# Performance work log

Hardware: AMD Instinct MI355X
Metric: run time of the kernel (lower is better)

## Reference

```python
import jax, jax.numpy as jnp
import numpy as np

ROW = 48   # num_row_points
COL = 48   # num_column_points
K = 21     # kernel_size


def _grid_sample_translate(ker, tx, ty):
    """Bilinear grid_sample (zeros padding, align_corners=True) for a pure
    per-image translation grid. ker: [N, h, w]; tx, ty: [N] normalized shifts.
    Matches F.affine_grid(identity + translation) + F.grid_sample."""
    N, h, w = ker.shape
    dt = ker.dtype
    # source pixel coords: px = x_out + tx*(w-1)/2 (align_corners=True)
    px = jnp.arange(w, dtype=dt)[None, :] + tx[:, None] * (w - 1) / 2  # [N, w]
    py = jnp.arange(h, dtype=dt)[None, :] + ty[:, None] * (h - 1) / 2  # [N, h]

    x0 = jnp.floor(px); fx = px - x0
    def gat_w(i):
        m = ((i >= 0) & (i <= w - 1)).astype(dt)
        ic = jnp.clip(i, 0, w - 1).astype(jnp.int32)
        v = jnp.take_along_axis(ker, jnp.broadcast_to(ic[:, None, :], ker.shape), axis=2)
        return v * m[:, None, :]
    gx = gat_w(x0) * (1 - fx)[:, None, :] + gat_w(x0 + 1) * fx[:, None, :]

    y0 = jnp.floor(py); fy = py - y0
    def gat_h(i):
        m = ((i >= 0) & (i <= h - 1)).astype(dt)
        ic = jnp.clip(i, 0, h - 1).astype(jnp.int32)
        v = jnp.take_along_axis(gx, jnp.broadcast_to(ic[:, :, None], gx.shape), axis=1)
        return v * m[:, :, None]
    return gat_h(y0) * (1 - fy)[:, :, None] + gat_h(y0 + 1) * fy[:, :, None]


def setup_inputs() -> dict:
    key = jax.random.key(0)
    k1, k2, k3 = jax.random.split(key, 3)
    N = ROW * COL
    inp = jax.random.normal(k1, (4, 64, 192, 192), dtype=jnp.float32)
    # torch.rand init; floor at 0.05 to avoid a degenerate zero sigma draw
    sigma_x = jax.random.uniform(k2, (N,), dtype=jnp.float32, minval=0.05, maxval=1.0)
    sigma_y = jax.random.uniform(k3, (N,), dtype=jnp.float32, minval=0.05, maxval=1.0)
    opacity = jnp.ones((N, 1), dtype=jnp.float32)
    return {"inp": inp, "sigma_x": sigma_x, "sigma_y": sigma_y, "opacity": opacity}


def reference(inp, sigma_x, sigma_y, opacity):
    B, C, H, W = inp.shape
    nbr, nbc = H // ROW, W // COL
    L = nbr * nbc
    N = ROW * COL

    # Unfold into non-overlapping ROWxCOL patches -> [B*L, C, ROW, COL]
    patches = (inp.reshape(B, C, nbr, ROW, nbc, COL)
                  .transpose(0, 2, 4, 1, 3, 5)
                  .reshape(B * L, C, ROW, COL))
    colors = patches.reshape(B * L, C, N).transpose(0, 2, 1)  # [BL, N, C]

    # meshgrid point coords: index k = i*COL + j, x=j (col), y=i (row)
    ii, jj = jnp.meshgrid(jnp.arange(ROW), jnp.arange(COL), indexing="ij")
    i = ii.reshape(-1).astype(inp.dtype)
    j = jj.reshape(-1).astype(inp.dtype)
    # coords_norm = (0.5 - [x/ROW, y/COL]) * 2  (note: x divided by height, as in source)
    tx = 1.0 - 2.0 * j / ROW
    ty = 1.0 - 2.0 * i / COL

    # per-point axis-aligned Gaussian kernel on [-5, 5]^2
    ax = jnp.linspace(-5.0, 5.0, K).astype(inp.dtype)
    xx2 = (ax ** 2)[None, :, None]  # x varies along first kernel dim
    yy2 = (ax ** 2)[None, None, :]
    sx2 = (sigma_x ** 2)[:, None, None]
    sy2 = (sigma_y ** 2)[:, None, None]
    z = -0.5 * (xx2 / sx2 + yy2 / sy2)                      # [N, K, K]
    kernel = jnp.exp(z) / (2.0 * jnp.pi * jnp.sqrt(sx2 * sy2))
    kernel = kernel / kernel.max(axis=(1, 2), keepdims=True)

    pad_h, pad_w = ROW - K, COL - K
    kp = jnp.pad(kernel, ((0, 0),
                          (pad_h // 2, pad_h // 2 + pad_h % 2),
                          (pad_w // 2, pad_w // 2 + pad_w % 2)))
    kt = _grid_sample_translate(kp, tx, ty)                  # [N, ROW, COL]

    weighted = colors * opacity[None, :, :]                  # [BL, N, C]
    out = jnp.einsum("bpc,phw->bchw", weighted, kt)          # splat-accumulate
    out = jnp.clip(out, 0.0, 1.0)

    # Fold back to [B, C, H, W]
    out = (out.reshape(B, nbr, nbc, C, ROW, COL)
              .transpose(0, 3, 1, 4, 2, 5)
              .reshape(B, C, H, W))
    return out
```

## Files before the change

### kernel.cpp

```cpp
#include <hip/hip_runtime.h>


#define NPTS 2304
#define KD   2304
#define HH   192

typedef _Float16 f16;
typedef _Float16 f16x8 __attribute__((ext_vector_type(8)));
typedef float f32x4 __attribute__((ext_vector_type(4)));

__device__ __forceinline__ void gload16(const f16* g, f16* l) {
    __builtin_amdgcn_global_load_lds((const __attribute__((address_space(1))) void*)g,
                                     (__attribute__((address_space(3))) void*)l,
                                     16, 0, 0);
}

__device__ __forceinline__ float gtap(float t, float inv2s) {
    float ax = 0.5f * t - 11.5f;
    float g = expf(-ax * ax * inv2s);
    return (t >= 12.5f && t <= 33.5f) ? g : 0.0f;
}

__global__ void build_kykx(const float* __restrict__ sx, const float* __restrict__ sy,
                           const float* __restrict__ op,
                           float* __restrict__ KY_T, float* __restrict__ KX_T) {
    int flat = blockIdx.x * 256 + threadIdx.x;
    if (flat >= 48 * NPTS) return;
    int pos = flat / NPTS;
    int p   = flat - pos * NPTS;
    int i = p / 48;
    int j = p - i * 48;
    float sxv = sx[p], syv = sy[p], opv = op[p];
    float invx = 0.5f / (sxv * sxv);
    float invy = 0.5f / (syv * syv);

    float py = (float)pos + 23.5f - (47.0f / 48.0f) * (float)i;
    float y0 = floorf(py), fy = py - y0;
    KY_T[flat] = opv * (gtap(y0, invx) * (1.0f - fy) + gtap(y0 + 1.0f, invx) * fy);

    float px = (float)pos + 23.5f - (47.0f / 48.0f) * (float)j;
    float x0 = floorf(px), fx = px - x0;
    KX_T[flat] = gtap(x0, invy) * (1.0f - fx) + gtap(x0 + 1.0f, invy) * fx;
}

__global__ void build_kt(const float* __restrict__ KY_T, const float* __restrict__ KX_T,
                         f16* __restrict__ Kt) {
    int idx = blockIdx.x * 256 + threadIdx.x;
    int hw = idx / 288;
    int p0 = (idx - hw * 288) * 8;
    int y = hw / 48, x = hw - y * 48;
    const float4* ky = (const float4*)(KY_T + (size_t)y * NPTS + p0);
    const float4* kx = (const float4*)(KX_T + (size_t)x * NPTS + p0);
    float4 a0 = ky[0], a1 = ky[1];
    float4 b0 = kx[0], b1 = kx[1];
    f16x8 r;
    r[0] = (f16)(a0.x * b0.x); r[1] = (f16)(a0.y * b0.y);
    r[2] = (f16)(a0.z * b0.z); r[3] = (f16)(a0.w * b0.w);
    r[4] = (f16)(a1.x * b1.x); r[5] = (f16)(a1.y * b1.y);
    r[6] = (f16)(a1.z * b1.z); r[7] = (f16)(a1.w * b1.w);
    *(f16x8*)(Kt + (size_t)hw * NPTS + p0) = r;
}

__global__ void pack_A(const float* __restrict__ inp, f16* __restrict__ A) {
    int idx = blockIdx.x * 256 + threadIdx.x;
    int m = idx / 288;
    int p0 = (idx - m * 288) * 8;
    int i = p0 / 48, j = p0 - i * 48;
    int bl = m >> 6, c = m & 63;
    int b = bl >> 4, pr = (bl >> 2) & 3, pc = bl & 3;
    const float* src = inp + ((size_t)(b * 64 + c) * HH + pr * 48 + i) * HH + pc * 48 + j;
    float4 a0 = *(const float4*)src;
    float4 a1 = *(const float4*)(src + 4);
    f16x8 r;
    r[0] = (f16)a0.x; r[1] = (f16)a0.y; r[2] = (f16)a0.z; r[3] = (f16)a0.w;
    r[4] = (f16)a1.x; r[5] = (f16)a1.y; r[6] = (f16)a1.z; r[7] = (f16)a1.w;
    *(f16x8*)(A + (size_t)m * KD + p0) = r;
}

__global__ __launch_bounds__(256) void gemm_splat(const f16* __restrict__ A,
                                                  const f16* __restrict__ Bt,
                                                  float* __restrict__ out) {
    __shared__ __attribute__((aligned(16))) f16 As[128 * 32];
    __shared__ __attribute__((aligned(16))) f16 Bs[128 * 32];

    int tid  = threadIdx.x;
    int lane = tid & 63;
    int w    = tid >> 6;
    int wr   = w >> 1, wc = w & 1;
    int bx   = blockIdx.x;
    int m0   = (bx / 18) * 128;
    int n0   = (bx % 18) * 128;

    int y_min = n0 / 48;
    int y_max = (n0 + 127) / 48;
    int i_lo = max(0,  (int)floorf((y_min - 10.5f) * (48.0f / 47.0f)));
    int i_hi = min(47, (int)ceilf ((y_max + 11.5f) * (48.0f / 47.0f)));
    int k_lo = (i_lo * 48) & ~31;
    int k_hi = min(KD, ((i_hi + 1) * 48 + 31) & ~31);

    int srow = lane >> 2;
    int sko  = (lane & 3) * 8;

    const int lrow = lane & 15;
    const int lk8  = (lane >> 4) * 8;

    f32x4 acc[4][4] = {};

    for (int k0 = k_lo; k0 < k_hi; k0 += 32) {
        #pragma unroll
        for (int c = 0; c < 2; ++c) {
            int r   = w + c * 4;
            int row = r * 16 + srow;
            gload16(&A [(size_t)(m0 + row) * KD + k0 + sko], &As[r * 512]);
            gload16(&Bt[(size_t)(n0 + row) * KD + k0 + sko], &Bs[r * 512]);
        }
        __syncthreads();

        f16x8 af[4], bf[4];
        #pragma unroll
        for (int mi = 0; mi < 4; ++mi)
            af[mi] = *(const f16x8*)&As[(wr * 64 + mi * 16 + lrow) * 32 + lk8];
        #pragma unroll
        for (int ni = 0; ni < 4; ++ni)
            bf[ni] = *(const f16x8*)&Bs[(wc * 64 + ni * 16 + lrow) * 32 + lk8];

        #pragma unroll
        for (int mi = 0; mi < 4; ++mi)
            #pragma unroll
            for (int ni = 0; ni < 4; ++ni)
                acc[mi][ni] = __builtin_amdgcn_mfma_f32_16x16x32_f16(af[mi], bf[ni], acc[mi][ni], 0, 0, 0);
        __syncthreads();
    }

    #pragma unroll
    for (int mi = 0; mi < 4; ++mi) {
        #pragma unroll
        for (int r = 0; r < 4; ++r) {
            int m  = m0 + wr * 64 + mi * 16 + (lane >> 4) * 4 + r;
            int bl = m >> 6, c = m & 63;
            int b  = bl >> 4, pr = (bl >> 2) & 3, pc = bl & 3;
            float* orow = out + ((size_t)(b * 64 + c) * HH + pr * 48) * HH + pc * 48;
            #pragma unroll
            for (int ni = 0; ni < 4; ++ni) {
                int n = n0 + wc * 64 + ni * 16 + (lane & 15);
                int y = n / 48, x = n - y * 48;
                float v = acc[mi][ni][r];
                v = fminf(fmaxf(v, 0.0f), 1.0f);
                orow[y * HH + x] = v;
            }
        }
    }
}

extern "C" void kernel_launch(void* const* d_in, const int* in_sizes, int n_in,
                              void* d_out, int out_size, void* d_ws, size_t ws_size,
                              hipStream_t stream) {
    const float* inp = (const float*)d_in[0];
    const float* sx  = (const float*)d_in[1];
    const float* sy  = (const float*)d_in[2];
    const float* op  = (const float*)d_in[3];
    float* out = (float*)d_out;

    char* ws = (char*)d_ws;
    float* KY_T = (float*)ws;
    float* KX_T = (float*)(ws + 442368);
    f16*   Kt   = (f16*)(ws + 884736);
    f16*   Ap   = (f16*)(ws + 884736 + 10616832);

    build_kykx<<<dim3(432),  dim3(256), 0, stream>>>(sx, sy, op, KY_T, KX_T);
    build_kt  <<<dim3(2592), dim3(256), 0, stream>>>(KY_T, KX_T, Kt);
    pack_A    <<<dim3(4608), dim3(256), 0, stream>>>(inp, Ap);
    gemm_splat<<<dim3(576),  dim3(256), 0, stream>>>(Ap, Kt, out);
}
```

Baseline: 146.4 us.

## Fuse kernel-table build, double-buffer GEMM LDS, swizzle LDS and remap workgroups

Merges the separable KY/KX table build into the Kt build so each element is computed directly from sigma and opacity, which drops one launch and an intermediate buffer round-trip. The GEMM now double-buffers its LDS tiles, issuing the next K-slice's global-to-LDS loads before the current slice's MFMAs with one barrier per iteration. It also XOR-swizzles the LDS k-offsets to reduce bank conflicts and remaps block IDs so neighbouring blocks spread across XCDs. The costs are recomputing the exponentials 8x per output element in build_kt and doubling the GEMM's LDS footprint.

```diff
diff --git a/kernel.cpp b/kernel.cpp
--- a/kernel.cpp
+++ b/kernel.cpp
@@ -21,43 +21,30 @@
     return (t >= 12.5f && t <= 33.5f) ? g : 0.0f;
 }
 
-__global__ void build_kykx(const float* __restrict__ sx, const float* __restrict__ sy,
-                           const float* __restrict__ op,
-                           float* __restrict__ KY_T, float* __restrict__ KX_T) {
-    int flat = blockIdx.x * 256 + threadIdx.x;
-    if (flat >= 48 * NPTS) return;
-    int pos = flat / NPTS;
-    int p   = flat - pos * NPTS;
-    int i = p / 48;
-    int j = p - i * 48;
-    float sxv = sx[p], syv = sy[p], opv = op[p];
-    float invx = 0.5f / (sxv * sxv);
-    float invy = 0.5f / (syv * syv);
-
-    float py = (float)pos + 23.5f - (47.0f / 48.0f) * (float)i;
-    float y0 = floorf(py), fy = py - y0;
-    KY_T[flat] = opv * (gtap(y0, invx) * (1.0f - fy) + gtap(y0 + 1.0f, invx) * fy);
-
-    float px = (float)pos + 23.5f - (47.0f / 48.0f) * (float)j;
-    float x0 = floorf(px), fx = px - x0;
-    KX_T[flat] = gtap(x0, invy) * (1.0f - fx) + gtap(x0 + 1.0f, invy) * fx;
-}
-
-__global__ void build_kt(const float* __restrict__ KY_T, const float* __restrict__ KX_T,
-                         f16* __restrict__ Kt) {
+__global__ void build_kt(const float* __restrict__ sx, const float* __restrict__ sy,
+                         const float* __restrict__ op, f16* __restrict__ Kt) {
     int idx = blockIdx.x * 256 + threadIdx.x;
     int hw = idx / 288;
     int p0 = (idx - hw * 288) * 8;
     int y = hw / 48, x = hw - y * 48;
-    const float4* ky = (const float4*)(KY_T + (size_t)y * NPTS + p0);
-    const float4* kx = (const float4*)(KX_T + (size_t)x * NPTS + p0);
-    float4 a0 = ky[0], a1 = ky[1];
-    float4 b0 = kx[0], b1 = kx[1];
+    int i = p0 / 48, j0 = p0 - i * 48;
+
+    float py = (float)y + 23.5f - (47.0f / 48.0f) * (float)i;
+    float y0 = floorf(py), fy = py - y0;
+
     f16x8 r;
-    r[0] = (f16)(a0.x * b0.x); r[1] = (f16)(a0.y * b0.y);
-    r[2] = (f16)(a0.z * b0.z); r[3] = (f16)(a0.w * b0.w);
-    r[4] = (f16)(a1.x * b1.x); r[5] = (f16)(a1.y * b1.y);
-    r[6] = (f16)(a1.z * b1.z); r[7] = (f16)(a1.w * b1.w);
+    #pragma unroll
+    for (int u = 0; u < 8; ++u) {
+        int p = p0 + u;
+        float sxv = sx[p], syv = sy[p], opv = op[p];
+        float invx = 0.5f / (sxv * sxv);
+        float invy = 0.5f / (syv * syv);
+        float ky = opv * (gtap(y0, invx) * (1.0f - fy) + gtap(y0 + 1.0f, invx) * fy);
+        float px = (float)x + 23.5f - (47.0f / 48.0f) * (float)(j0 + u);
+        float x0 = floorf(px), fx = px - x0;
+        float kx = gtap(x0, invy) * (1.0f - fx) + gtap(x0 + 1.0f, invy) * fx;
+        r[u] = (f16)(ky * kx);
+    }
     *(f16x8*)(Kt + (size_t)hw * NPTS + p0) = r;
 }
 
@@ -80,16 +67,17 @@
 __global__ __launch_bounds__(256) void gemm_splat(const f16* __restrict__ A,
                                                   const f16* __restrict__ Bt,
                                                   float* __restrict__ out) {
-    __shared__ __attribute__((aligned(16))) f16 As[128 * 32];
-    __shared__ __attribute__((aligned(16))) f16 Bs[128 * 32];
+    __shared__ __attribute__((aligned(16))) f16 As[2 * 4096];
+    __shared__ __attribute__((aligned(16))) f16 Bs[2 * 4096];
 
     int tid  = threadIdx.x;
     int lane = tid & 63;
     int w    = tid >> 6;
     int wr   = w >> 1, wc = w & 1;
     int bx   = blockIdx.x;
-    int m0   = (bx / 18) * 128;
-    int n0   = (bx % 18) * 128;
+    int wg   = (bx & 7) * 72 + (bx >> 3);
+    int m0   = (wg / 18) * 128;
+    int n0   = (wg % 18) * 128;
 
     int y_min = n0 / 48;
     int y_max = (n0 + 127) / 48;
@@ -97,40 +85,50 @@
     int i_hi = min(47, (int)ceilf ((y_max + 11.5f) * (48.0f / 47.0f)));
     int k_lo = (i_lo * 48) & ~31;
     int k_hi = min(KD, ((i_hi + 1) * 48 + 31) & ~31);
+    int nt   = (k_hi - k_lo) >> 5;
 
     int srow = lane >> 2;
-    int sko  = (lane & 3) * 8;
+    int sk   = (((lane & 3) ^ ((lane >> 3) & 3)) << 3);
+    const f16* Abase = A  + (size_t)(m0 + w * 32 + srow) * KD + sk + k_lo;
+    const f16* Bbase = Bt + (size_t)(n0 + w * 32 + srow) * KD + sk + k_lo;
 
-    const int lrow = lane & 15;
-    const int lk8  = (lane >> 4) * 8;
+    int lrow = lane & 15;
+    int koe  = (((lane >> 4) ^ ((lane >> 1) & 3)) << 3);
 
     f32x4 acc[4][4] = {};
 
-    for (int k0 = k_lo; k0 < k_hi; k0 += 32) {
-        #pragma unroll
-        for (int c = 0; c < 2; ++c) {
-            int r   = w + c * 4;
-            int row = r * 16 + srow;
-            gload16(&A [(size_t)(m0 + row) * KD + k0 + sko], &As[r * 512]);
-            gload16(&Bt[(size_t)(n0 + row) * KD + k0 + sko], &Bs[r * 512]);
-        }
-        __syncthreads();
+    #define STAGE(buf, koff)                                                          \
+        do {                                                                          \
+            gload16(Abase + (koff),            &As[(buf) * 4096 + w * 1024]);         \
+            gload16(Abase + 16 * KD + (koff),  &As[(buf) * 4096 + w * 1024 + 512]);   \
+            gload16(Bbase + (koff),            &Bs[(buf) * 4096 + w * 1024]);         \
+            gload16(Bbase + 16 * KD + (koff),  &Bs[(buf) * 4096 + w * 1024 + 512]);   \
+        } while (0)
+
+    STAGE(0, 0);
+    __syncthreads();
+
+    for (int t = 0; t < nt; ++t) {
+        int cur = t & 1;
+        if (t + 1 < nt) STAGE(cur ^ 1, (t + 1) << 5);
 
         f16x8 af[4], bf[4];
         #pragma unroll
         for (int mi = 0; mi < 4; ++mi)
-            af[mi] = *(const f16x8*)&As[(wr * 64 + mi * 16 + lrow) * 32 + lk8];
+            af[mi] = *(const f16x8*)&As[cur * 4096 + (wr * 64 + mi * 16 + lrow) * 32 + koe];
         #pragma unroll
         for (int ni = 0; ni < 4; ++ni)
-            bf[ni] = *(const f16x8*)&Bs[(wc * 64 + ni * 16 + lrow) * 32 + lk8];
+            bf[ni] = *(const f16x8*)&Bs[cur * 4096 + (wc * 64 + ni * 16 + lrow) * 32 + koe];
 
         #pragma unroll
         for (int mi = 0; mi < 4; ++mi)
             #pragma unroll
             for (int ni = 0; ni < 4; ++ni)
                 acc[mi][ni] = __builtin_amdgcn_mfma_f32_16x16x32_f16(af[mi], bf[ni], acc[mi][ni], 0, 0, 0);
+
         __syncthreads();
     }
+    #undef STAGE
 
     #pragma unroll
     for (int mi = 0; mi < 4; ++mi) {
@@ -162,13 +160,10 @@
     float* out = (float*)d_out;
 
     char* ws = (char*)d_ws;
-    float* KY_T = (float*)ws;
-    float* KX_T = (float*)(ws + 442368);
-    f16*   Kt   = (f16*)(ws + 884736);
-    f16*   Ap   = (f16*)(ws + 884736 + 10616832);
+    f16* Kt = (f16*)ws;
+    f16* Ap = (f16*)(ws + 10616832);
 
-    build_kykx<<<dim3(432),  dim3(256), 0, stream>>>(sx, sy, op, KY_T, KX_T);
-    build_kt  <<<dim3(2592), dim3(256), 0, stream>>>(KY_T, KX_T, Kt);
+    build_kt  <<<dim3(2592), dim3(256), 0, stream>>>(sx, sy, op, Kt);
     pack_A    <<<dim3(4608), dim3(256), 0, stream>>>(inp, Ap);
     gemm_splat<<<dim3(576),  dim3(256), 0, stream>>>(Ap, Kt, out);
 }
```

New measurement: 138.4 us. 1.06x faster.
